# Performance work log

Hardware: AMD Instinct MI355X
Metric: run time of the kernel (lower is better)

Reference implementation:

```python
import jax, jax.numpy as jnp
import numpy as np

DIM = 192
HEADS = 6
WS = 8
SHIFT = 4
POS_DIM = 12  # (dim//4)//4
HIDDEN = 768
EPS = 1e-5


def _win_partition(x, ws):
    B, H, W, C = x.shape
    x = x.reshape(B, H // ws, ws, W // ws, ws, C)
    return x.transpose(0, 1, 3, 2, 4, 5).reshape(-1, ws, ws, C)


def _win_reverse(w, ws, H, W):
    B = w.shape[0] // ((H // ws) * (W // ws))
    x = w.reshape(B, H // ws, W // ws, ws, ws, -1)
    return x.transpose(0, 1, 3, 2, 4, 5).reshape(B, H, W, -1)


def _calc_mask(H, W, ws, shift):
    img = np.zeros((1, H, W, 1), np.float32)
    sl = (slice(0, -ws), slice(-ws, -shift), slice(-shift, None))
    cnt = 0
    for hs in sl:
        for wsl in sl:
            img[:, hs, wsl, :] = cnt
            cnt += 1
    mw = img.reshape(1, H // ws, ws, W // ws, ws, 1).transpose(0, 1, 3, 2, 4, 5).reshape(-1, ws * ws)
    am = mw[:, None, :] - mw[:, :, None]
    am = np.where(am != 0, -100.0, 0.0).astype(np.float32)
    return am  # [nW, N, N]


def _rel_index(ws):
    coords = np.stack(np.meshgrid(np.arange(ws), np.arange(ws), indexing='ij')).reshape(2, -1)
    rel = (coords[:, :, None] - coords[:, None, :]).transpose(1, 2, 0)
    rel[..., 0] += ws - 1
    rel[..., 1] += ws - 1
    rel[..., 0] *= 2 * ws - 1
    return rel.sum(-1)  # [N, N]


def _biases(ws):
    bh = np.arange(1 - ws, ws)
    bw = np.arange(1 - ws, ws)
    b = np.stack(np.meshgrid(bh, bw, indexing='ij')).reshape(2, -1).T
    return b.astype(np.float32)  # [(2ws-1)^2, 2]


def _ln(x, g, b):
    mu = jnp.mean(x, -1, keepdims=True)
    var = jnp.var(x, -1, keepdims=True)
    return (x - mu) / jnp.sqrt(var + EPS) * g + b


def setup_inputs() -> dict:
    key = jax.random.key(0)
    ks = jax.random.split(key, 20)
    B, L, C = 8, 128 * 128, DIM
    d = {
        'x': jax.random.normal(ks[0], (B, L, C), jnp.float32),
        'k_v': jnp.zeros((1,), jnp.float32),
        'H': 128, 'W': 128,
        'n1_g': jnp.ones((C,)), 'n1_b': jnp.zeros((C,)),
        'qkv_w': jax.random.normal(ks[1], (C, 3 * C)) * 0.02,
        'qkv_b': jnp.zeros((3 * C,)),
        'proj_w': jax.random.normal(ks[2], (C, C)) * 0.02,
        'proj_b': jnp.zeros((C,)),
        'pp_w': jax.random.normal(ks[3], (2, POS_DIM)) * 0.02,
        'pp_b': jnp.zeros((POS_DIM,)),
        'p1_g': jnp.ones((POS_DIM,)), 'p1_b': jnp.zeros((POS_DIM,)),
        'p1_w': jax.random.normal(ks[4], (POS_DIM, POS_DIM)) * 0.02,
        'p1_bias': jnp.zeros((POS_DIM,)),
        'p2_g': jnp.ones((POS_DIM,)), 'p2_b': jnp.zeros((POS_DIM,)),
        'p2_w': jax.random.normal(ks[5], (POS_DIM, POS_DIM)) * 0.02,
        'p2_bias': jnp.zeros((POS_DIM,)),
        'p3_g': jnp.ones((POS_DIM,)), 'p3_b': jnp.zeros((POS_DIM,)),
        'p3_w': jax.random.normal(ks[6], (POS_DIM, HEADS)) * 0.02,
        'p3_bias': jnp.zeros((HEADS,)),
        'n2_g': jnp.ones((C,)), 'n2_b': jnp.zeros((C,)),
        'fc1_w': jax.random.normal(ks[7], (C, HIDDEN)) * 0.02,
        'fc1_b': jnp.zeros((HIDDEN,)),
        'fc2_w': jax.random.normal(ks[8], (HIDDEN, C)) * 0.02,
        'fc2_b': jnp.zeros((C,)),
    }
    return d


def reference(x, k_v, H, W, n1_g, n1_b, qkv_w, qkv_b, proj_w, proj_b,
              pp_w, pp_b, p1_g, p1_b, p1_w, p1_bias, p2_g, p2_b, p2_w, p2_bias,
              p3_g, p3_b, p3_w, p3_bias, n2_g, n2_b, fc1_w, fc1_b, fc2_w, fc2_b):
    B, L, C = x.shape
    N = WS * WS
    hd = C // HEADS
    scale = hd ** (-0.5)

    rel_idx = jnp.asarray(_rel_index(WS).reshape(-1))            # [N*N]
    biases = jnp.asarray(_biases(WS))                            # [(2WS-1)^2, 2]
    mask = jnp.asarray(_calc_mask(H, W, WS, SHIFT))              # [nW, N, N]

    shortcut = x
    h = _ln(x, n1_g, n1_b).reshape(B, H, W, C)
    h = jnp.roll(h, (-SHIFT, -SHIFT), (1, 2))
    xw = _win_partition(h, WS).reshape(-1, N, C)                 # [B*nW, N, C]
    B_ = xw.shape[0]

    qkv = (xw @ qkv_w + qkv_b).reshape(B_, N, 3, HEADS, hd).transpose(2, 0, 3, 1, 4)
    q, k, v = qkv[0] * scale, qkv[1], qkv[2]                     # [B_, H, N, hd]
    attn = jnp.einsum('bhnd,bhmd->bhnm', q, k)

    # dynamic position bias MLP (residual=False path)
    pos = biases @ pp_w + pp_b
    pos = jax.nn.relu(_ln(pos, p1_g, p1_b)) @ p1_w + p1_bias
    pos = jax.nn.relu(_ln(pos, p2_g, p2_b)) @ p2_w + p2_bias
    pos = jax.nn.relu(_ln(pos, p3_g, p3_b)) @ p3_w + p3_bias     # [(2WS-1)^2, HEADS]
    rpb = pos[rel_idx].reshape(N, N, HEADS).transpose(2, 0, 1)   # [HEADS, N, N]
    attn = attn + rpb[None]

    nW = mask.shape[0]
    attn = attn.reshape(B_ // nW, nW, HEADS, N, N) + mask[None, :, None]
    attn = jax.nn.softmax(attn.reshape(-1, HEADS, N, N), axis=-1)

    out = jnp.einsum('bhnm,bhmd->bhnd', attn, v).transpose(0, 2, 1, 3).reshape(B_, N, C)
    out = out @ proj_w + proj_b

    out = _win_reverse(out.reshape(-1, WS, WS, C), WS, H, W)
    out = jnp.roll(out, (SHIFT, SHIFT), (1, 2)).reshape(B, L, C)

    y = shortcut + out
    m = _ln(y, n2_g, n2_b)
    m = jax.nn.gelu(m @ fc1_w + fc1_b, approximate=False) @ fc2_w + fc2_b
    return y + m
```

## Files before the change

kernel.cpp:

```cpp
#include <hip/hip_runtime.h>
#include <hip/hip_bf16.h>
#include <math.h>

using bf16 = __hip_bfloat16;

typedef __bf16 bf16x8 __attribute__((ext_vector_type(8)));
typedef float f32x4 __attribute__((ext_vector_type(4)));

__device__ __forceinline__ float bf2f(bf16 v) { return __bfloat162float(v); }
__device__ __forceinline__ bf16 f2bf(float v) { return __float2bfloat16(v); }
__device__ __forceinline__ float nz(float v) { return (v == v) ? v : 0.0f; }

__device__ __forceinline__ void gload_lds16(const void* g, void* l) {
    __builtin_amdgcn_global_load_lds(
        (const __attribute__((address_space(1))) unsigned int*)g,
        (__attribute__((address_space(3))) unsigned int*)l, 16, 0, 0);
}

#define CDIM 192
#define NHEADS 6
#define ROWS 131072
#define HIDDEN 768

__global__ __launch_bounds__(256) void k_ln1_part(const float* __restrict__ x,
                                                  const float* __restrict__ g,
                                                  const float* __restrict__ bta,
                                                  bf16* __restrict__ xw) {
    int tid = threadIdx.x;
    int lane = tid & 63;
    int t = (blockIdx.x << 2) + (tid >> 6);
    int w = t >> 6, n = t & 63;
    int bb = w >> 8, wy = (w >> 4) & 15, wx = w & 15;
    int iy = n >> 3, ix = n & 7;
    int hs = (wy * 8 + iy + 4) & 127;
    int vs = (wx * 8 + ix + 4) & 127;
    const float* xr = x + ((size_t)bb * 16384 + (size_t)hs * 128 + vs) * CDIM;
    float v0 = nz(xr[lane]);
    float v1 = nz(xr[lane + 64]);
    float v2 = nz(xr[lane + 128]);
    float s = v0 + v1 + v2;
    float q = v0 * v0 + v1 * v1 + v2 * v2;
#pragma unroll
    for (int o = 32; o > 0; o >>= 1) { s += __shfl_xor(s, o); q += __shfl_xor(q, o); }
    float mean = s * (1.0f / 192.0f);
    float var = q * (1.0f / 192.0f) - mean * mean;
    float rs = rsqrtf(var + 1e-5f);
    bf16* orow = xw + (size_t)t * CDIM;
    orow[lane]       = f2bf((v0 - mean) * rs * g[lane]       + bta[lane]);
    orow[lane + 64]  = f2bf((v1 - mean) * rs * g[lane + 64]  + bta[lane + 64]);
    orow[lane + 128] = f2bf((v2 - mean) * rs * g[lane + 128] + bta[lane + 128]);
}

__global__ void k_transpose(const float* __restrict__ in, bf16* __restrict__ out, int K, int N) {
    int i = blockIdx.x * 256 + threadIdx.x;
    if (i < K * N) {
        int k = i / N, n = i - k * N;
        out[(size_t)n * K + k] = f2bf(in[i]);
    }
}

__global__ __launch_bounds__(256) void k_posmlp(
    const float* __restrict__ pp_w, const float* __restrict__ pp_b,
    const float* __restrict__ p1_g, const float* __restrict__ p1_b,
    const float* __restrict__ p1_w, const float* __restrict__ p1_bias,
    const float* __restrict__ p2_g, const float* __restrict__ p2_b,
    const float* __restrict__ p2_w, const float* __restrict__ p2_bias,
    const float* __restrict__ p3_g, const float* __restrict__ p3_b,
    const float* __restrict__ p3_w, const float* __restrict__ p3_bias,
    float* __restrict__ pos) {
    int i = threadIdx.x;
    if (i >= 225) return;
    float bh = (float)(i / 15 - 7), bw = (float)(i % 15 - 7);
    float v[12], u[12];
#pragma unroll
    for (int j = 0; j < 12; j++)
        v[j] = bh * pp_w[j] + bw * pp_w[12 + j] + pp_b[j];

    auto stage = [&](const float* gg, const float* bb2, const float* Wm, const float* bs, int OD) {
        float mean = 0.f;
        for (int j = 0; j < 12; j++) mean += v[j];
        mean *= (1.0f / 12.0f);
        float var = 0.f;
        for (int j = 0; j < 12; j++) { float d = v[j] - mean; var += d * d; }
        var *= (1.0f / 12.0f);
        float rs = rsqrtf(var + 1e-5f);
        for (int j = 0; j < 12; j++)
            u[j] = fmaxf((v[j] - mean) * rs * gg[j] + bb2[j], 0.0f);
        for (int o = 0; o < OD; o++) {
            float a = bs[o];
            for (int j = 0; j < 12; j++) a += u[j] * Wm[j * OD + o];
            v[o] = a;
        }
    };
    stage(p1_g, p1_b, p1_w, p1_bias, 12);
    stage(p2_g, p2_b, p2_w, p2_bias, 12);
    stage(p3_g, p3_b, p3_w, p3_bias, 6);
    for (int h = 0; h < 6; h++) pos[i * 6 + h] = v[h];
}

template <int ACT, int RESID, typename OutT>
__global__ __launch_bounds__(256) void k_gemm(const bf16* __restrict__ A,
                                              const bf16* __restrict__ Bt,
                                              const float* __restrict__ bias,
                                              OutT* __restrict__ Cd,
                                              int M, int N, int K) {
    constexpr int BM = 128, BN = 64, BK = 64;
    __shared__ __align__(16) unsigned short As[2][BM * BK];
    __shared__ __align__(16) unsigned short Bs[2][BN * BK];
    int tid = threadIdx.x;
    int wv = tid >> 6, lane = tid & 63;
    int lm = lane & 15, quad = lane >> 4;
    int sub = lane >> 3;
    int cb8 = (((lane & 7) ^ sub) << 3);
    int n0 = blockIdx.x * BN;
    int m0 = blockIdx.y * BM;

    const bf16* aSrc = A  + (size_t)(m0 + wv * 32 + sub) * K + cb8;
    const bf16* bSrc = Bt + (size_t)(n0 + wv * 16 + sub) * K + cb8;

    auto stage = [&](int buf, int k0) {
#pragma unroll
        for (int i = 0; i < 4; ++i)
            gload_lds16(aSrc + (size_t)(i * 8) * K + k0,
                        &As[buf][(wv * 32 + i * 8) * 64]);
#pragma unroll
        for (int i = 0; i < 2; ++i)
            gload_lds16(bSrc + (size_t)(i * 8) * K + k0,
                        &Bs[buf][(wv * 16 + i * 8) * 64]);
    };

    f32x4 acc[2][4] = {};

    auto compute = [&](int buf) {
#pragma unroll
        for (int ks = 0; ks < BK; ks += 32) {
            int xk = (ks + quad * 8) ^ ((lm & 7) << 3);
            bf16x8 af[2], bq[4];
#pragma unroll
            for (int im = 0; im < 2; ++im)
                af[im] = *(const bf16x8*)&As[buf][(wv * 32 + im * 16 + lm) * 64 + xk];
#pragma unroll
            for (int in = 0; in < 4; ++in)
                bq[in] = *(const bf16x8*)&Bs[buf][(in * 16 + lm) * 64 + xk];
#pragma unroll
            for (int im = 0; im < 2; ++im)
#pragma unroll
                for (int in = 0; in < 4; ++in)
                    acc[im][in] = __builtin_amdgcn_mfma_f32_16x16x32_bf16(
                        af[im], bq[in], acc[im][in], 0, 0, 0);
        }
    };

    const int nt = K / BK;
    stage(0, 0);
    if (nt > 1) stage(1, BK);
    int cur = 0;
    for (int t = 0; t < nt; ++t) {
        if (t + 1 < nt)
            asm volatile("s_waitcnt vmcnt(6)" ::: "memory");
        else
            asm volatile("s_waitcnt vmcnt(0)" ::: "memory");
        __builtin_amdgcn_s_barrier();
        compute(cur);
        if (t + 2 < nt) {
            __builtin_amdgcn_s_barrier();
            stage(cur, (t + 2) * BK);
        }
        cur ^= 1;
    }

#pragma unroll
    for (int im = 0; im < 2; ++im) {
        int rbase = m0 + wv * 32 + im * 16 + quad * 4;
#pragma unroll
        for (int in = 0; in < 4; ++in) {
            int cg = n0 + in * 16 + lm;
            float bv = bias[cg];
#pragma unroll
            for (int r = 0; r < 4; ++r) {
                float v = acc[im][in][r] + bv;
                if (ACT == 1) v = 0.5f * v * (1.0f + erff(v * 0.70710678118654752f));
                size_t o = (size_t)(rbase + r) * N + cg;
                if (RESID) v += (float)Cd[o];
                Cd[o] = (OutT)v;
            }
        }
    }
}

__global__ __launch_bounds__(256) void k_attn(const bf16* __restrict__ qkv,
                                              const float* __restrict__ pos,
                                              bf16* __restrict__ outp) {
    __shared__ __align__(16) unsigned short Qs[64 * 40];
    __shared__ __align__(16) unsigned short Ks[64 * 40];
    __shared__ __align__(16) unsigned short Vt[32 * 72];
    __shared__ __align__(16) unsigned short Ps[64 * 72];
    int w = blockIdx.x, tid = threadIdx.x;
    int wv = tid >> 6, lane = tid & 63;
    int lm = lane & 15, quad = lane >> 4;
    int wy = (w >> 4) & 15, wx = w & 15;
    bool edge = (wy == 15) || (wx == 15);
    const float scale = 0.17677669529663687f;

    int srow = tid >> 2, scol = (tid & 3) << 3;
    const unsigned short* gq =
        (const unsigned short*)qkv + ((size_t)w * 64 + srow) * 576 + scol;

    int nbase = wv * 16 + quad * 4;

    for (int h = 0; h < 6; ++h) {
        uint4 uq = *(const uint4*)(gq + h * 32);
        uint4 uk = *(const uint4*)(gq + h * 32 + 192);
        uint4 uv = *(const uint4*)(gq + h * 32 + 384);
        *(uint4*)&Qs[srow * 40 + scol] = uq;
        *(uint4*)&Ks[srow * 40 + scol] = uk;
        const unsigned short* pv = (const unsigned short*)&uv;
#pragma unroll
        for (int j = 0; j < 8; j++) Vt[(scol + j) * 72 + srow] = pv[j];
        __syncthreads();

        f32x4 acc[4];
        bf16x8 af = *(const bf16x8*)&Qs[(wv * 16 + lm) * 40 + quad * 8];
#pragma unroll
        for (int ct = 0; ct < 4; ++ct) {
            bf16x8 bfk = *(const bf16x8*)&Ks[(ct * 16 + lm) * 40 + quad * 8];
            f32x4 z = {0.f, 0.f, 0.f, 0.f};
            acc[ct] = __builtin_amdgcn_mfma_f32_16x16x32_bf16(af, bfk, z, 0, 0, 0);
        }

        float sv[4][4];
#pragma unroll
        for (int ct = 0; ct < 4; ++ct) {
            int m = ct * 16 + lm;
            int iym = m >> 3, ixm = m & 7;
            int hm = wy * 8 + iym, wm = wx * 8 + ixm;
            int ridm = (hm < 120 ? 0 : (hm < 124 ? 1 : 2)) * 3 +
                       (wm < 120 ? 0 : (wm < 124 ? 1 : 2));
#pragma unroll
            for (int r = 0; r < 4; r++) {
                int n = nbase + r;
                int iyn = n >> 3, ixn = n & 7;
                float s = acc[ct][r] * scale +
                          pos[((iyn - iym + 7) * 15 + (ixn - ixm + 7)) * 6 + h];
                if (edge) {
                    int hn = wy * 8 + iyn, wn = wx * 8 + ixn;
                    int ridn = (hn < 120 ? 0 : (hn < 124 ? 1 : 2)) * 3 +
                               (wn < 120 ? 0 : (wn < 124 ? 1 : 2));
                    if (ridn != ridm) s -= 100.0f;
                }
                sv[ct][r] = s;
            }
        }

#pragma unroll
        for (int r = 0; r < 4; r++) {
            float mx = fmaxf(fmaxf(sv[0][r], sv[1][r]), fmaxf(sv[2][r], sv[3][r]));
#pragma unroll
            for (int o = 1; o < 16; o <<= 1) mx = fmaxf(mx, __shfl_xor(mx, o));
            float e0 = expf(sv[0][r] - mx), e1 = expf(sv[1][r] - mx);
            float e2 = expf(sv[2][r] - mx), e3 = expf(sv[3][r] - mx);
            float sum = e0 + e1 + e2 + e3;
#pragma unroll
            for (int o = 1; o < 16; o <<= 1) sum += __shfl_xor(sum, o);
            float inv = 1.0f / sum;
            int n = nbase + r;
            *(bf16*)&Ps[n * 72 + lm]      = f2bf(e0 * inv);
            *(bf16*)&Ps[n * 72 + 16 + lm] = f2bf(e1 * inv);
            *(bf16*)&Ps[n * 72 + 32 + lm] = f2bf(e2 * inv);
            *(bf16*)&Ps[n * 72 + 48 + lm] = f2bf(e3 * inv);
        }
        __syncthreads();

        f32x4 o0 = {0.f, 0.f, 0.f, 0.f}, o1 = {0.f, 0.f, 0.f, 0.f};
#pragma unroll
        for (int kc = 0; kc < 2; kc++) {
            bf16x8 pa = *(const bf16x8*)&Ps[(wv * 16 + lm) * 72 + kc * 32 + quad * 8];
            bf16x8 vb0 = *(const bf16x8*)&Vt[lm * 72 + kc * 32 + quad * 8];
            bf16x8 vb1 = *(const bf16x8*)&Vt[(16 + lm) * 72 + kc * 32 + quad * 8];
            o0 = __builtin_amdgcn_mfma_f32_16x16x32_bf16(pa, vb0, o0, 0, 0, 0);
            o1 = __builtin_amdgcn_mfma_f32_16x16x32_bf16(pa, vb1, o1, 0, 0, 0);
        }
#pragma unroll
        for (int r = 0; r < 4; r++) {
            int n = nbase + r;
            size_t base = ((size_t)w * 64 + n) * 192 + h * 32;
            outp[base + lm]      = f2bf(o0[r]);
            outp[base + 16 + lm] = f2bf(o1[r]);
        }
        __syncthreads();
    }
}

__global__ __launch_bounds__(256) void k_resid_ln2(const float* __restrict__ x,
                                                   const bf16* __restrict__ proj,
                                                   const float* __restrict__ g,
                                                   const float* __restrict__ bta,
                                                   float* __restrict__ yout,
                                                   bf16* __restrict__ h2) {
    int tid = threadIdx.x, lane = tid & 63;
    int t = (blockIdx.x << 2) + (tid >> 6);
    int bb = t >> 14, l = t & 16383;
    int h = l >> 7, ww = l & 127;
    int hr = (h + 124) & 127, wr = (ww + 124) & 127;
    int win = bb * 256 + (hr >> 3) * 16 + (wr >> 3);
    int n = ((hr & 7) << 3) + (wr & 7);
    const float* xr = x + (size_t)t * CDIM;
    const bf16* pr = proj + ((size_t)win * 64 + n) * CDIM;
    float v0 = nz(xr[lane])       + bf2f(pr[lane]);
    float v1 = nz(xr[lane + 64])  + bf2f(pr[lane + 64]);
    float v2 = nz(xr[lane + 128]) + bf2f(pr[lane + 128]);
    float* yr = yout + (size_t)t * CDIM;
    yr[lane]       = v0;
    yr[lane + 64]  = v1;
    yr[lane + 128] = v2;
    float s = v0 + v1 + v2;
    float q = v0 * v0 + v1 * v1 + v2 * v2;
#pragma unroll
    for (int o = 32; o > 0; o >>= 1) { s += __shfl_xor(s, o); q += __shfl_xor(q, o); }
    float mean = s * (1.0f / 192.0f);
    float var = q * (1.0f / 192.0f) - mean * mean;
    float rs = rsqrtf(var + 1e-5f);
    bf16* hr2 = h2 + (size_t)t * CDIM;
    hr2[lane]       = f2bf((v0 - mean) * rs * g[lane]       + bta[lane]);
    hr2[lane + 64]  = f2bf((v1 - mean) * rs * g[lane + 64]  + bta[lane + 64]);
    hr2[lane + 128] = f2bf((v2 - mean) * rs * g[lane + 128] + bta[lane + 128]);
}

extern "C" void kernel_launch(void* const* d_in, const int* in_sizes, int n_in,
                              void* d_out, int out_size, void* d_ws, size_t ws_size,
                              hipStream_t stream) {
    (void)in_sizes; (void)n_in; (void)out_size;
    const float* x      = (const float*)d_in[0];
    const float* n1_g   = (const float*)d_in[4];
    const float* n1_b   = (const float*)d_in[5];
    const float* qkv_w  = (const float*)d_in[6];
    const float* qkv_b  = (const float*)d_in[7];
    const float* proj_w = (const float*)d_in[8];
    const float* proj_b = (const float*)d_in[9];
    const float* pp_w   = (const float*)d_in[10];
    const float* pp_b   = (const float*)d_in[11];
    const float* p1_g   = (const float*)d_in[12];
    const float* p1_b   = (const float*)d_in[13];
    const float* p1_w   = (const float*)d_in[14];
    const float* p1_bias= (const float*)d_in[15];
    const float* p2_g   = (const float*)d_in[16];
    const float* p2_b   = (const float*)d_in[17];
    const float* p2_w   = (const float*)d_in[18];
    const float* p2_bias= (const float*)d_in[19];
    const float* p3_g   = (const float*)d_in[20];
    const float* p3_b   = (const float*)d_in[21];
    const float* p3_w   = (const float*)d_in[22];
    const float* p3_bias= (const float*)d_in[23];
    const float* n2_g   = (const float*)d_in[24];
    const float* n2_b   = (const float*)d_in[25];
    const float* fc1_w  = (const float*)d_in[26];
    const float* fc1_b  = (const float*)d_in[27];
    const float* fc2_w  = (const float*)d_in[28];
    const float* fc2_b  = (const float*)d_in[29];

    char* ws = (char*)d_ws;
    size_t off = 0;
    auto alloc = [&](size_t bytes) -> char* {
        char* p = ws + off;
        off += (bytes + 255) & ~(size_t)255;
        return p;
    };
    bf16* qkvwT  = (bf16*)alloc((size_t)CDIM * 576 * 2);
    bf16* projwT = (bf16*)alloc((size_t)CDIM * CDIM * 2);
    bf16* fc1wT  = (bf16*)alloc((size_t)CDIM * HIDDEN * 2);
    bf16* fc2wT  = (bf16*)alloc((size_t)HIDDEN * CDIM * 2);
    float* pos   = (float*)alloc(225 * 6 * 4);

    const size_t flatNeed = (size_t)ROWS * CDIM * 2 + (size_t)ROWS * HIDDEN * 2 + (1u << 20);
    const bool flat = (ws_size > off) && ((ws_size - off) >= flatNeed);
    const int NCH = flat ? 1 : 8;
    const int NIMG = flat ? 8 : 1;
    const size_t R = (size_t)16384 * NIMG;

    bf16 *xw_b, *qkv_buf, *attn_b, *proj_buf, *h2_b, *fc1_buf;
    if (flat) {
        bf16* region0 = (bf16*)alloc((size_t)ROWS * CDIM * 2);
        bf16* region1 = (bf16*)alloc((size_t)ROWS * HIDDEN * 2);
        xw_b = attn_b = h2_b = region0;
        qkv_buf  = region1;
        proj_buf = region1 + (size_t)ROWS * 576;
        fc1_buf  = region1;
    } else {
        xw_b     = (bf16*)alloc(R * CDIM * 2);
        qkv_buf  = (bf16*)alloc(R * 576 * 2);
        attn_b   = (bf16*)alloc(R * CDIM * 2);
        proj_buf = (bf16*)alloc(R * CDIM * 2);
        h2_b     = (bf16*)alloc(R * CDIM * 2);
        fc1_buf  = (bf16*)alloc(R * HIDDEN * 2);
    }
    float* yout = (float*)d_out;

    k_transpose<<<(CDIM * 576 + 255) / 256, 256, 0, stream>>>(qkv_w, qkvwT, CDIM, 576);
    k_transpose<<<(CDIM * CDIM + 255) / 256, 256, 0, stream>>>(proj_w, projwT, CDIM, CDIM);
    k_transpose<<<(CDIM * HIDDEN + 255) / 256, 256, 0, stream>>>(fc1_w, fc1wT, CDIM, HIDDEN);
    k_transpose<<<(HIDDEN * CDIM + 255) / 256, 256, 0, stream>>>(fc2_w, fc2wT, HIDDEN, CDIM);
    k_posmlp<<<1, 256, 0, stream>>>(pp_w, pp_b, p1_g, p1_b, p1_w, p1_bias,
                                    p2_g, p2_b, p2_w, p2_bias,
                                    p3_g, p3_b, p3_w, p3_bias, pos);

    for (int c = 0; c < NCH; ++c) {
        const float* x_c = x + (size_t)c * 16384 * CDIM;
        float* y_c = yout + (size_t)c * 16384 * CDIM;

        k_ln1_part<<<(int)(R / 4), 256, 0, stream>>>(x_c, n1_g, n1_b, xw_b);

        k_gemm<0, 0, bf16><<<dim3(576 / 64, (int)(R / 128)), 256, 0, stream>>>(
            xw_b, qkvwT, qkv_b, qkv_buf, (int)R, 576, CDIM);

        k_attn<<<(int)(R / 64), 256, 0, stream>>>(qkv_buf, pos, attn_b);

        k_gemm<0, 0, bf16><<<dim3(CDIM / 64, (int)(R / 128)), 256, 0, stream>>>(
            attn_b, projwT, proj_b, proj_buf, (int)R, CDIM, CDIM);

        k_resid_ln2<<<(int)(R / 4), 256, 0, stream>>>(x_c, proj_buf, n2_g, n2_b, y_c, h2_b);

        k_gemm<1, 0, bf16><<<dim3(HIDDEN / 64, (int)(R / 128)), 256, 0, stream>>>(
            h2_b, fc1wT, fc1_b, fc1_buf, (int)R, HIDDEN, CDIM);

        k_gemm<0, 1, float><<<dim3(CDIM / 64, (int)(R / 128)), 256, 0, stream>>>(
            fc1_buf, fc2wT, fc2_b, y_c, (int)R, CDIM, HIDDEN);
    }
}
```

Baseline: 731.2 us.

## Widen GEMM tile to full 192 columns and fuse residual+LN2 into proj epilogue

The GEMM N-tile grows from 64 to 192 columns, so each block covers a full row of C=192 outputs and reuses each A tile across more columns. With full rows available, the projection GEMM epilogue now does the window-reverse/roll scatter, residual add, and LayerNorm2 via 16-lane shuffles. This removes the separate k_resid_ln2 kernel and the proj_buf round trip. The cost is 96 accumulator VGPRs per thread and larger LDS, which may lower occupancy, fewer blocks in the grid, and a dedicated h2 buffer in the flat layout.

```diff
diff --git a/kernel.cpp b/kernel.cpp
--- a/kernel.cpp
+++ b/kernel.cpp
@@ -98,13 +98,18 @@
     for (int h = 0; h < 6; h++) pos[i * 6 + h] = v[h];
 }
 
-template <int ACT, int RESID, typename OutT>
+template <int EPI, typename OutT>
 __global__ __launch_bounds__(256) void k_gemm(const bf16* __restrict__ A,
                                               const bf16* __restrict__ Bt,
                                               const float* __restrict__ bias,
                                               OutT* __restrict__ Cd,
-                                              int M, int N, int K) {
-    constexpr int BM = 128, BN = 64, BK = 64;
+                                              int M, int N, int K,
+                                              const float* __restrict__ xres,
+                                              const float* __restrict__ g2,
+                                              const float* __restrict__ b2,
+                                              float* __restrict__ yout,
+                                              bf16* __restrict__ h2out) {
+    constexpr int BM = 128, BN = 192, BK = 64;
     __shared__ __align__(16) unsigned short As[2][BM * BK];
     __shared__ __align__(16) unsigned short Bs[2][BN * BK];
     int tid = threadIdx.x;
@@ -116,7 +121,7 @@
     int m0 = blockIdx.y * BM;
 
     const bf16* aSrc = A  + (size_t)(m0 + wv * 32 + sub) * K + cb8;
-    const bf16* bSrc = Bt + (size_t)(n0 + wv * 16 + sub) * K + cb8;
+    const bf16* bSrc = Bt + (size_t)(n0 + wv * 48 + sub) * K + cb8;
 
     auto stage = [&](int buf, int k0) {
 #pragma unroll
@@ -124,40 +129,39 @@
             gload_lds16(aSrc + (size_t)(i * 8) * K + k0,
                         &As[buf][(wv * 32 + i * 8) * 64]);
 #pragma unroll
-        for (int i = 0; i < 2; ++i)
+        for (int i = 0; i < 6; ++i)
             gload_lds16(bSrc + (size_t)(i * 8) * K + k0,
-                        &Bs[buf][(wv * 16 + i * 8) * 64]);
+                        &Bs[buf][(wv * 48 + i * 8) * 64]);
     };
 
-    f32x4 acc[2][4] = {};
+    f32x4 acc[2][12] = {};
 
     auto compute = [&](int buf) {
 #pragma unroll
         for (int ks = 0; ks < BK; ks += 32) {
             int xk = (ks + quad * 8) ^ ((lm & 7) << 3);
-            bf16x8 af[2], bq[4];
+            bf16x8 af[2];
 #pragma unroll
             for (int im = 0; im < 2; ++im)
                 af[im] = *(const bf16x8*)&As[buf][(wv * 32 + im * 16 + lm) * 64 + xk];
 #pragma unroll
-            for (int in = 0; in < 4; ++in)
-                bq[in] = *(const bf16x8*)&Bs[buf][(in * 16 + lm) * 64 + xk];
-#pragma unroll
-            for (int im = 0; im < 2; ++im)
-#pragma unroll
-                for (int in = 0; in < 4; ++in)
+            for (int in = 0; in < 12; ++in) {
+                bf16x8 bq = *(const bf16x8*)&Bs[buf][(in * 16 + lm) * 64 + xk];
+#pragma unroll
+                for (int im = 0; im < 2; ++im)
                     acc[im][in] = __builtin_amdgcn_mfma_f32_16x16x32_bf16(
-                        af[im], bq[in], acc[im][in], 0, 0, 0);
+                        af[im], bq, acc[im][in], 0, 0, 0);
+            }
         }
     };
 
     const int nt = K / BK;
     stage(0, 0);
-    if (nt > 1) stage(1, BK);
+    stage(1, BK);
     int cur = 0;
     for (int t = 0; t < nt; ++t) {
         if (t + 1 < nt)
-            asm volatile("s_waitcnt vmcnt(6)" ::: "memory");
+            asm volatile("s_waitcnt vmcnt(10)" ::: "memory");
         else
             asm volatile("s_waitcnt vmcnt(0)" ::: "memory");
         __builtin_amdgcn_s_barrier();
@@ -169,20 +173,71 @@
         cur ^= 1;
     }
 
-#pragma unroll
-    for (int im = 0; im < 2; ++im) {
-        int rbase = m0 + wv * 32 + im * 16 + quad * 4;
-#pragma unroll
-        for (int in = 0; in < 4; ++in) {
-            int cg = n0 + in * 16 + lm;
-            float bv = bias[cg];
+    if (EPI == 0 || EPI == 1) {
+#pragma unroll
+        for (int im = 0; im < 2; ++im) {
+            int rbase = m0 + wv * 32 + im * 16 + quad * 4;
+#pragma unroll
+            for (int in = 0; in < 12; ++in) {
+                int cg = n0 + in * 16 + lm;
+                float bv = bias[cg];
+#pragma unroll
+                for (int r = 0; r < 4; ++r) {
+                    float v = acc[im][in][r] + bv;
+                    if (EPI == 1) v = 0.5f * v * (1.0f + erff(v * 0.70710678118654752f));
+                    Cd[(size_t)(rbase + r) * N + cg] = (OutT)v;
+                }
+            }
+        }
+    } else if (EPI == 2) {
+#pragma unroll
+        for (int im = 0; im < 2; ++im) {
+            int rbase = m0 + wv * 32 + im * 16 + quad * 4;
+#pragma unroll
+            for (int in = 0; in < 12; ++in) {
+                int cg = in * 16 + lm;
+                float bv = bias[cg];
+#pragma unroll
+                for (int r = 0; r < 4; ++r) {
+                    size_t o = (size_t)(rbase + r) * 192 + cg;
+                    yout[o] = acc[im][in][r] + bv + yout[o];
+                }
+            }
+        }
+    } else {
+#pragma unroll
+        for (int im = 0; im < 2; ++im) {
+            int rbase = m0 + wv * 32 + im * 16 + quad * 4;
 #pragma unroll
             for (int r = 0; r < 4; ++r) {
-                float v = acc[im][in][r] + bv;
-                if (ACT == 1) v = 0.5f * v * (1.0f + erff(v * 0.70710678118654752f));
-                size_t o = (size_t)(rbase + r) * N + cg;
-                if (RESID) v += (float)Cd[o];
-                Cd[o] = (OutT)v;
+                int grow = rbase + r;
+                int w = grow >> 6, n = grow & 63;
+                int bb = w >> 8, wy = (w >> 4) & 15, wx = w & 15;
+                int iy = n >> 3, ix = n & 7;
+                int hs = (wy * 8 + iy + 4) & 127;
+                int vs = (wx * 8 + ix + 4) & 127;
+                size_t xrow = ((size_t)bb * 16384 + (size_t)hs * 128 + vs) * 192;
+                float vv[12];
+                float s = 0.f, q = 0.f;
+#pragma unroll
+                for (int in = 0; in < 12; ++in) {
+                    int col = in * 16 + lm;
+                    float v = acc[im][in][r] + bias[col] + nz(xres[xrow + col]);
+                    yout[xrow + col] = v;
+                    vv[in] = v; s += v; q += v * v;
+                }
+#pragma unroll
+                for (int o = 1; o < 16; o <<= 1) {
+                    s += __shfl_xor(s, o); q += __shfl_xor(q, o);
+                }
+                float mean = s * (1.0f / 192.0f);
+                float var = q * (1.0f / 192.0f) - mean * mean;
+                float rsv = rsqrtf(var + 1e-5f);
+#pragma unroll
+                for (int in = 0; in < 12; ++in) {
+                    int col = in * 16 + lm;
+                    h2out[xrow + col] = f2bf((vv[in] - mean) * rsv * g2[col] + b2[col]);
+                }
             }
         }
     }
@@ -289,41 +344,6 @@
         }
         __syncthreads();
     }
-}
-
-__global__ __launch_bounds__(256) void k_resid_ln2(const float* __restrict__ x,
-                                                   const bf16* __restrict__ proj,
-                                                   const float* __restrict__ g,
-                                                   const float* __restrict__ bta,
-                                                   float* __restrict__ yout,
-                                                   bf16* __restrict__ h2) {
-    int tid = threadIdx.x, lane = tid & 63;
-    int t = (blockIdx.x << 2) + (tid >> 6);
-    int bb = t >> 14, l = t & 16383;
-    int h = l >> 7, ww = l & 127;
-    int hr = (h + 124) & 127, wr = (ww + 124) & 127;
-    int win = bb * 256 + (hr >> 3) * 16 + (wr >> 3);
-    int n = ((hr & 7) << 3) + (wr & 7);
-    const float* xr = x + (size_t)t * CDIM;
-    const bf16* pr = proj + ((size_t)win * 64 + n) * CDIM;
-    float v0 = nz(xr[lane])       + bf2f(pr[lane]);
-    float v1 = nz(xr[lane + 64])  + bf2f(pr[lane + 64]);
-    float v2 = nz(xr[lane + 128]) + bf2f(pr[lane + 128]);
-    float* yr = yout + (size_t)t * CDIM;
-    yr[lane]       = v0;
-    yr[lane + 64]  = v1;
-    yr[lane + 128] = v2;
-    float s = v0 + v1 + v2;
-    float q = v0 * v0 + v1 * v1 + v2 * v2;
-#pragma unroll
-    for (int o = 32; o > 0; o >>= 1) { s += __shfl_xor(s, o); q += __shfl_xor(q, o); }
-    float mean = s * (1.0f / 192.0f);
-    float var = q * (1.0f / 192.0f) - mean * mean;
-    float rs = rsqrtf(var + 1e-5f);
-    bf16* hr2 = h2 + (size_t)t * CDIM;
-    hr2[lane]       = f2bf((v0 - mean) * rs * g[lane]       + bta[lane]);
-    hr2[lane + 64]  = f2bf((v1 - mean) * rs * g[lane + 64]  + bta[lane + 64]);
-    hr2[lane + 128] = f2bf((v2 - mean) * rs * g[lane + 128] + bta[lane + 128]);
 }
 
 extern "C" void kernel_launch(void* const* d_in, const int* in_sizes, int n_in,
@@ -371,25 +391,27 @@
     bf16* fc2wT  = (bf16*)alloc((size_t)HIDDEN * CDIM * 2);
     float* pos   = (float*)alloc(225 * 6 * 4);
 
-    const size_t flatNeed = (size_t)ROWS * CDIM * 2 + (size_t)ROWS * HIDDEN * 2 + (1u << 20);
+    const size_t flatNeed = (size_t)ROWS * CDIM * 2
+                          + (size_t)ROWS * HIDDEN * 2
+                          + (size_t)ROWS * CDIM * 2
+                          + (1u << 20);
     const bool flat = (ws_size > off) && ((ws_size - off) >= flatNeed);
     const int NCH = flat ? 1 : 8;
     const int NIMG = flat ? 8 : 1;
     const size_t R = (size_t)16384 * NIMG;
 
-    bf16 *xw_b, *qkv_buf, *attn_b, *proj_buf, *h2_b, *fc1_buf;
+    bf16 *xw_b, *qkv_buf, *attn_b, *h2_b, *fc1_buf;
     if (flat) {
         bf16* region0 = (bf16*)alloc((size_t)ROWS * CDIM * 2);
         bf16* region1 = (bf16*)alloc((size_t)ROWS * HIDDEN * 2);
-        xw_b = attn_b = h2_b = region0;
-        qkv_buf  = region1;
-        proj_buf = region1 + (size_t)ROWS * 576;
-        fc1_buf  = region1;
+        h2_b = (bf16*)alloc((size_t)ROWS * CDIM * 2);
+        xw_b = attn_b = region0;
+        qkv_buf = region1;
+        fc1_buf = region1;
     } else {
         xw_b     = (bf16*)alloc(R * CDIM * 2);
         qkv_buf  = (bf16*)alloc(R * 576 * 2);
         attn_b   = (bf16*)alloc(R * CDIM * 2);
-        proj_buf = (bf16*)alloc(R * CDIM * 2);
         h2_b     = (bf16*)alloc(R * CDIM * 2);
         fc1_buf  = (bf16*)alloc(R * HIDDEN * 2);
     }
@@ -409,20 +431,22 @@
 
         k_ln1_part<<<(int)(R / 4), 256, 0, stream>>>(x_c, n1_g, n1_b, xw_b);
 
-        k_gemm<0, 0, bf16><<<dim3(576 / 64, (int)(R / 128)), 256, 0, stream>>>(
-            xw_b, qkvwT, qkv_b, qkv_buf, (int)R, 576, CDIM);
+        k_gemm<0, bf16><<<dim3(576 / 192, (int)(R / 128)), 256, 0, stream>>>(
+            xw_b, qkvwT, qkv_b, qkv_buf, (int)R, 576, CDIM,
+            nullptr, nullptr, nullptr, nullptr, nullptr);
 
         k_attn<<<(int)(R / 64), 256, 0, stream>>>(qkv_buf, pos, attn_b);
 
-        k_gemm<0, 0, bf16><<<dim3(CDIM / 64, (int)(R / 128)), 256, 0, stream>>>(
-            attn_b, projwT, proj_b, proj_buf, (int)R, CDIM, CDIM);
-
-        k_resid_ln2<<<(int)(R / 4), 256, 0, stream>>>(x_c, proj_buf, n2_g, n2_b, y_c, h2_b);
-
-        k_gemm<1, 0, bf16><<<dim3(HIDDEN / 64, (int)(R / 128)), 256, 0, stream>>>(
-            h2_b, fc1wT, fc1_b, fc1_buf, (int)R, HIDDEN, CDIM);
-
-        k_gemm<0, 1, float><<<dim3(CDIM / 64, (int)(R / 128)), 256, 0, stream>>>(
-            fc1_buf, fc2wT, fc2_b, y_c, (int)R, CDIM, HIDDEN);
-    }
-}
+        k_gemm<3, bf16><<<dim3(1, (int)(R / 128)), 256, 0, stream>>>(
+            attn_b, projwT, proj_b, (bf16*)nullptr, (int)R, CDIM, CDIM,
+            x_c, n2_g, n2_b, y_c, h2_b);
+
+        k_gemm<1, bf16><<<dim3(HIDDEN / 192, (int)(R / 128)), 256, 0, stream>>>(
+            h2_b, fc1wT, fc1_b, fc1_buf, (int)R, HIDDEN, CDIM,
+            nullptr, nullptr, nullptr, nullptr, nullptr);
+
+        k_gemm<2, float><<<dim3(1, (int)(R / 128)), 256, 0, stream>>>(
+            fc1_buf, fc2wT, fc2_b, y_c, (int)R, CDIM, HIDDEN,
+            nullptr, nullptr, nullptr, y_c, nullptr);
+    }
+}
```

After: 677.4 us. 7.4% less time.
